# Kernel optimization log

Measured on AMD Instinct MI355X. Metric: run time of the kernel, lower is better.

## Reference

```python
import jax, jax.numpy as jnp
import numpy as np

B, T, D = 64, 512, 128          # batch, time, input_dim
S = 16                           # num_sessions
P, STRIDE = 3, 1                 # patch size / stride
H = 512                          # hidden_size
HORIZONS = (1, 5, 10)
K = len(HORIZONS)
TOK = D * P                      # token_dim = 384
EPS = 1e-6


def setup_inputs() -> dict:
    key = jax.random.key(0)
    ks = jax.random.split(key, 16)
    s = 0.02
    return {
        "x": jax.random.normal(ks[0], (B, T, D), jnp.float32),
        "session_idx": jax.random.randint(ks[1], (B,), 0, S),
        # per-session affine (expert) params
        "sess_W": jax.random.normal(ks[2], (S, D, D), jnp.float32) * s,
        "sess_b": jax.random.normal(ks[3], (S, D), jnp.float32) * s,
        # projection token_dim -> hidden
        "proj_W": jax.random.normal(ks[4], (H, TOK), jnp.float32) * s,
        "proj_b": jax.random.normal(ks[5], (H,), jnp.float32) * s,
        "rms_scale": jnp.ones((H,), jnp.float32),
        # single-layer GRU params (PyTorch layout: [3H, in], gate order r,z,n)
        "gru_Wih": jax.random.normal(ks[6], (3 * H, H), jnp.float32) * s,
        "gru_Whh": jax.random.normal(ks[7], (3 * H, H), jnp.float32) * s,
        "gru_bih": jax.random.normal(ks[8], (3 * H,), jnp.float32) * s,
        "gru_bhh": jax.random.normal(ks[9], (3 * H,), jnp.float32) * s,
        # future heads (K horizons): Linear(H,H) -> GELU -> Linear(H,TOK)
        "head_W1": jax.random.normal(ks[10], (K, H, H), jnp.float32) * s,
        "head_b1": jax.random.normal(ks[11], (K, H), jnp.float32) * s,
        "head_W2": jax.random.normal(ks[12], (K, TOK, H), jnp.float32) * s,
        "head_b2": jax.random.normal(ks[13], (K, TOK), jnp.float32) * s,
    }


def _forward(x, session_idx, sess_W, sess_b, proj_W, proj_b, rms_scale,
             gru_Wih, gru_Whh, gru_bih, gru_bhh,
             head_W1, head_b1, head_W2, head_b2):
    # --- per-sample session affine (expert gather + batched GEMM) ---
    W = sess_W[session_idx]                      # [B, D, D]
    b = sess_b[session_idx]                      # [B, D]
    aligned = jnp.einsum('btd,bed->bte', x, W) + b[:, None, :]  # y = x @ W.T + b

    # --- patch unfold along time; torch unfold gives [N, D, P] -> flatten (d,p) ---
    N = (T - P) // STRIDE + 1
    idx = jnp.arange(N)[:, None] * STRIDE + jnp.arange(P)[None, :]  # [N, P]
    win = aligned[:, idx, :]                     # [B, N, P, D]
    tokens = jnp.transpose(win, (0, 1, 3, 2)).reshape(B, N, TOK)    # [B, N, D*P]

    # --- projection + RMSNorm ---
    h = tokens @ proj_W.T + proj_b               # [B, N, H]
    rms = jnp.sqrt(jnp.mean(h * h, axis=-1, keepdims=True) + EPS)
    h = h / rms * rms_scale

    # --- GRU (PyTorch gate order r, z, n) via lax.scan over time ---
    gx = h @ gru_Wih.T + gru_bih                 # [B, N, 3H], precomputed input gates
    gx_t = jnp.transpose(gx, (1, 0, 2))          # [N, B, 3H]

    def step(hprev, g):
        gh = hprev @ gru_Whh.T + gru_bhh         # [B, 3H]
        r = jax.nn.sigmoid(g[:, :H] + gh[:, :H])
        z = jax.nn.sigmoid(g[:, H:2 * H] + gh[:, H:2 * H])
        n = jnp.tanh(g[:, 2 * H:] + r * gh[:, 2 * H:])
        hn = (1.0 - z) * n + z * hprev
        return hn, hn

    h0 = jnp.zeros((B, H), h.dtype)
    _, hs = jax.lax.scan(step, h0, gx_t)         # [N, B, H]
    hidden = jnp.transpose(hs, (1, 0, 2))        # [B, N, H]

    # --- multi-head future MLPs (stacked over K horizons) ---
    a = jnp.einsum('bnh,kfh->kbnf', hidden, head_W1) + head_b1[:, None, None, :]
    a = jax.nn.gelu(a, approximate=False)        # torch nn.GELU default = exact
    preds = jnp.einsum('kbnf,ktf->kbnt', a, head_W2) + head_b2[:, None, None, :]
    return preds, tokens                          # preds: [K, B, N, TOK]


def reference(x, session_idx, sess_W, sess_b, proj_W, proj_b, rms_scale,
              gru_Wih, gru_Whh, gru_bih, gru_bhh,
              head_W1, head_b1, head_W2, head_b2):
    return _forward(x, session_idx, sess_W, sess_b, proj_W, proj_b, rms_scale,
                    gru_Wih, gru_Whh, gru_bih, gru_bhh,
                    head_W1, head_b1, head_W2, head_b2)
```

## Files before the change

kernel.cpp:

```cpp
#include <hip/hip_runtime.h>
#include <hip/hip_bf16.h>
#include <math.h>

typedef __hip_bfloat16 bf16;
typedef __attribute__((ext_vector_type(8))) short short8;
typedef __attribute__((ext_vector_type(4))) short short4v;
typedef __attribute__((ext_vector_type(4))) float f32x4;

#define B_    64
#define T_    512
#define D_    128
#define N_    510
#define H_    512
#define TOK_  384
#define PRED1_ 12533760L
#define TOKOFF_ 37601280L

#define O_XBF  0UL
#define O_SWB  8388608UL
#define O_PW   8912896UL
#define O_WIH  9306112UL
#define O_WHH  10878976UL
#define O_W1   12451840UL
#define O_W2   14024704UL
#define O_TOK  15204352UL
#define O_HBF  40271872UL
#define O_HID  73695232UL
#define O_ABF  107118592UL
#define O_GX   140541952UL

__global__ void k_f2b(const float* __restrict__ s, bf16* __restrict__ d, int n4) {
  int i = blockIdx.x * 256 + threadIdx.x;
  if (i < n4) {
    float4 v = ((const float4*)s)[i];
    union { short4v sv; bf16 h[4]; } u;
    u.h[0] = __float2bfloat16(v.x); u.h[1] = __float2bfloat16(v.y);
    u.h[2] = __float2bfloat16(v.z); u.h[3] = __float2bfloat16(v.w);
    ((short4v*)d)[i] = u.sv;
  }
}

enum { EPI_F32 = 0, EPI_BF16 = 1, EPI_GELU = 2, EPI_TOK = 3, EPI_F32R = 4 };
#define SLDA 40

template <int EPI>
__global__ __launch_bounds__(256, 2) void k_gemm(
    const bf16* __restrict__ A, const bf16* __restrict__ W,
    const float* __restrict__ bias, void* __restrict__ C,
    int K, int ldc, long zA, long zW, long zB, long zC,
    const int* __restrict__ sidx, float* __restrict__ tokf, bf16* __restrict__ tokb)
{
  const int tid = threadIdx.x;
  const int bm = blockIdx.x, bn = blockIdx.y, z = blockIdx.z;
  const int wsel = (EPI == EPI_TOK) ? sidx[z] : z;
  const int lane = tid & 63, wave = tid >> 6;
  const int wm = (wave & 1) << 6, wn = (wave >> 1) << 6;
  const int r16 = lane & 15, quad = lane >> 4;

  __shared__ bf16 sA[128 * SLDA];
  __shared__ bf16 sB[128 * SLDA];

  const bf16* Ag = A + (long)z * zA + (long)bm * 128 * K;
  const bf16* Wg = W + (long)wsel * zW + (long)bn * 128 * K;

  f32x4 zf = {0.f, 0.f, 0.f, 0.f};
  f32x4 acc[4][4];
  for (int i = 0; i < 4; ++i) for (int j = 0; j < 4; ++j) acc[i][j] = zf;

  const int sr = tid >> 1, sc = (tid & 1) << 4;
  for (int k0 = 0; k0 < K; k0 += 32) {
    *(short8*)&sA[sr*SLDA + sc]     = *(const short8*)&Ag[(long)sr*K + k0 + sc];
    *(short8*)&sA[sr*SLDA + sc + 8] = *(const short8*)&Ag[(long)sr*K + k0 + sc + 8];
    *(short8*)&sB[sr*SLDA + sc]     = *(const short8*)&Wg[(long)sr*K + k0 + sc];
    *(short8*)&sB[sr*SLDA + sc + 8] = *(const short8*)&Wg[(long)sr*K + k0 + sc + 8];
    __syncthreads();
    short8 fa[4], fb[4];
    for (int i = 0; i < 4; ++i) fa[i] = *(const short8*)&sA[(wm + i*16 + r16)*SLDA + quad*8];
    for (int j = 0; j < 4; ++j) fb[j] = *(const short8*)&sB[(wn + j*16 + r16)*SLDA + quad*8];
    for (int i = 0; i < 4; ++i)
      for (int j = 0; j < 4; ++j)
        acc[i][j] = __builtin_amdgcn_mfma_f32_16x16x32_bf16(fa[i], fb[j], acc[i][j], 0, 0, 0);
    __syncthreads();
  }

  const float* bz = bias + (long)wsel * zB + bn * 128;
  for (int i = 0; i < 4; ++i) {
    for (int j = 0; j < 4; ++j) {
      const int colL = wn + j*16 + r16;
      const float bv = bz[colL];
      for (int r = 0; r < 4; ++r) {
        float v = acc[i][j][r] + bv;
        const long grow = (long)bm*128 + wm + i*16 + quad*4 + r;
        const long gcol = (long)bn*128 + colL;
        if (EPI == EPI_F32) {
          ((float*)C)[(long)z*zC + grow*ldc + gcol] = v;
        } else if (EPI == EPI_BF16) {
          ((bf16*)C)[(long)z*zC + grow*ldc + gcol] = __float2bfloat16(v);
        } else if (EPI == EPI_GELU) {
          v = 0.5f * v * (1.0f + erff(v * 0.70710678118654752f));
          ((bf16*)C)[(long)z*zC + grow*ldc + gcol] = __float2bfloat16(v);
        } else if (EPI == EPI_F32R) {
          const long rb = grow & 63, rn = grow >> 6;
          ((float*)C)[(rb*510 + rn)*ldc + gcol] = v;
        } else {
          for (int p = 0; p < 3; ++p) {
            long n = grow - p;
            if (n >= 0 && n < N_) {
              tokf[((long)z*N_ + n)*TOK_ + gcol*3 + p] = v;
              tokb[((long)n*B_ + z)*TOK_ + gcol*3 + p] = __float2bfloat16(v);
            }
          }
        }
      }
    }
  }
}

__global__ __launch_bounds__(256) void k_rms(const float* __restrict__ hpre,
                                             const float* __restrict__ scale,
                                             bf16* __restrict__ hbf)
{
  const int wave = threadIdx.x >> 6, lane = threadIdx.x & 63;
  const long row = (long)blockIdx.x * 4 + wave;
  const float* p = hpre + row * 512 + lane * 8;
  float4 v0 = *(const float4*)p;
  float4 v1 = *(const float4*)(p + 4);
  float ss = v0.x*v0.x + v0.y*v0.y + v0.z*v0.z + v0.w*v0.w
           + v1.x*v1.x + v1.y*v1.y + v1.z*v1.z + v1.w*v1.w;
  for (int m = 32; m >= 1; m >>= 1) ss += __shfl_xor(ss, m, 64);
  const float inv = 1.0f / sqrtf(ss * (1.0f/512.0f) + 1e-6f);
  const float* sc = scale + lane * 8;
  union { short8 sv; bf16 h[8]; } u;
  u.h[0] = __float2bfloat16(v0.x*inv*sc[0]); u.h[1] = __float2bfloat16(v0.y*inv*sc[1]);
  u.h[2] = __float2bfloat16(v0.z*inv*sc[2]); u.h[3] = __float2bfloat16(v0.w*inv*sc[3]);
  u.h[4] = __float2bfloat16(v1.x*inv*sc[4]); u.h[5] = __float2bfloat16(v1.y*inv*sc[5]);
  u.h[6] = __float2bfloat16(v1.z*inv*sc[6]); u.h[7] = __float2bfloat16(v1.w*inv*sc[7]);
  *(short8*)(hbf + row * 512 + lane * 8) = u.sv;
}

#define KP 520

#define GL2LDS(g, l) __builtin_amdgcn_global_load_lds( \
    (const __attribute__((address_space(1))) void*)(g), \
    (__attribute__((address_space(3))) void*)(l), 16, 0, 16)

__global__ __launch_bounds__(64, 1) void k_gru(
    const bf16* __restrict__ gx,
    const bf16* __restrict__ Whh,
    const float* __restrict__ bhh,
    bf16* __restrict__ hidden,
    int* __restrict__ flags)
{
  const int lane = threadIdx.x & 63;
  const int c16  = lane & 15, quad = lane >> 4;
  const int pw   = blockIdx.x & 31;
  const int gb   = blockIdx.x >> 5;
  const int hwv  = pw * 16;
  const int b0   = gb * 8;

  __shared__ bf16 wlds[16 * 3 * 64 * 8];
  __shared__ bf16 hp[8 * KP];

  for (int g3 = 0; g3 < 3; ++g3)
    for (int kt = 0; kt < 16; ++kt)
      *(short8*)&wlds[((kt*3 + g3)*64 + lane)*8] =
          *(const short8*)&Whh[(long)(g3*512 + hwv + c16)*512 + kt*32 + quad*8];
  const float bhr = bhh[       hwv + c16];
  const float bhz = bhh[ 512 + hwv + c16];
  const float bhn = bhh[1024 + hwv + c16];
  __syncthreads();

  int* myflag = &flags[(gb*32 + pw) * 32];
  const int pidx = (gb*32 + (lane & 31)) * 32;
  const int brv = (quad & 1) * 4;

  float gr[4], gz[4], gn[4];
  float hcur[4] = {0.f, 0.f, 0.f, 0.f};
  {
    const bf16* gxs = gx + (long)b0 * 1536 + hwv + c16;
#pragma unroll
    for (int i2 = 0; i2 < 4; ++i2) {
      const long ro = (long)(brv + i2) * 1536;
      gr[i2] = __bfloat162float(gxs[ro]);
      gz[i2] = __bfloat162float(gxs[ro + 512]);
      gn[i2] = __bfloat162float(gxs[ro + 1024]);
    }
  }

  for (int s = 0; s < 510; ++s) {
    f32x4 ar = {0.f,0.f,0.f,0.f}, az = {0.f,0.f,0.f,0.f}, an = {0.f,0.f,0.f,0.f};

    if (s > 0) {
      while (true) {
        int fv = __hip_atomic_load(&flags[pidx], __ATOMIC_RELAXED, __HIP_MEMORY_SCOPE_AGENT);
        if (__all(fv >= s)) break;
        __builtin_amdgcn_s_sleep(1);
      }
      asm volatile("" ::: "memory");

      const bf16* src = hidden + ((long)(s-1)*64 + b0)*512 + lane*8;
#pragma unroll
      for (int b = 0; b < 8; ++b) GL2LDS(src + b*512, &hp[b*KP]);
      asm volatile("s_waitcnt vmcnt(0)" ::: "memory");

#pragma unroll
      for (int kt = 0; kt < 16; ++kt) {
        short8 a  = *(const short8*)&hp[(c16 & 7)*KP + kt*32 + quad*8];
        short8 fr = *(const short8*)&wlds[((kt*3 + 0)*64 + lane)*8];
        short8 fz = *(const short8*)&wlds[((kt*3 + 1)*64 + lane)*8];
        short8 fn = *(const short8*)&wlds[((kt*3 + 2)*64 + lane)*8];
        ar = __builtin_amdgcn_mfma_f32_16x16x32_bf16(a, fr, ar, 0, 0, 0);
        az = __builtin_amdgcn_mfma_f32_16x16x32_bf16(a, fz, az, 0, 0, 0);
        an = __builtin_amdgcn_mfma_f32_16x16x32_bf16(a, fn, an, 0, 0, 0);
      }
    }

    if (quad < 2) {
#pragma unroll
      for (int i2 = 0; i2 < 4; ++i2) {
        const float r  = 1.0f / (1.0f + expf(-(gr[i2] + ar[i2] + bhr)));
        const float z  = 1.0f / (1.0f + expf(-(gz[i2] + az[i2] + bhz)));
        const float nn = tanhf(gn[i2] + r * (an[i2] + bhn));
        const float hn = (1.0f - z)*nn + z*hcur[i2];
        union { bf16 h; unsigned short u; } cb; cb.h = __float2bfloat16(hn);
        hcur[i2] = __bfloat162float(cb.h);
        unsigned mine = cb.u;
        unsigned part = (unsigned)__shfl_xor((int)mine, 1, 64);
        if (!(c16 & 1)) {
          unsigned w = (part << 16) | mine;
          __hip_atomic_store((unsigned*)(hidden + ((long)s*64 + b0 + brv + i2)*512 + hwv + c16),
                             w, __ATOMIC_RELAXED, __HIP_MEMORY_SCOPE_AGENT);
        }
      }
    }
    if (s < 509) {
      asm volatile("s_waitcnt vmcnt(0)" ::: "memory");
      if (lane == 0)
        __hip_atomic_store(myflag, s + 1, __ATOMIC_RELAXED, __HIP_MEMORY_SCOPE_AGENT);
      asm volatile("" ::: "memory");
      const bf16* gxs = gx + ((long)(s+1)*64 + b0)*1536 + hwv + c16;
#pragma unroll
      for (int i2 = 0; i2 < 4; ++i2) {
        const long ro = (long)(brv + i2) * 1536;
        gr[i2] = __bfloat162float(gxs[ro]);
        gz[i2] = __bfloat162float(gxs[ro + 512]);
        gn[i2] = __bfloat162float(gxs[ro + 1024]);
      }
    }
  }
}

extern "C" void kernel_launch(void* const* d_in, const int* in_sizes, int n_in,
                              void* d_out, int out_size, void* d_ws, size_t ws_size,
                              hipStream_t stream)
{
  const float* x    = (const float*)d_in[0];
  const int*   sidx = (const int*)d_in[1];
  const float* sW   = (const float*)d_in[2];
  const float* sb   = (const float*)d_in[3];
  const float* pW   = (const float*)d_in[4];
  const float* pb   = (const float*)d_in[5];
  const float* rsc  = (const float*)d_in[6];
  const float* wih  = (const float*)d_in[7];
  const float* whh  = (const float*)d_in[8];
  const float* bih  = (const float*)d_in[9];
  const float* bhh  = (const float*)d_in[10];
  const float* w1   = (const float*)d_in[11];
  const float* b1   = (const float*)d_in[12];
  const float* w2   = (const float*)d_in[13];
  const float* b2   = (const float*)d_in[14];
  char* ws = (char*)d_ws;
  float* out = (float*)d_out;

  bf16* xbf   = (bf16*)(ws + O_XBF);
  bf16* swbf  = (bf16*)(ws + O_SWB);
  bf16* pwbf  = (bf16*)(ws + O_PW);
  bf16* wihbf = (bf16*)(ws + O_WIH);
  bf16* whhbf = (bf16*)(ws + O_WHH);
  bf16* w1bf  = (bf16*)(ws + O_W1);
  bf16* w2bf  = (bf16*)(ws + O_W2);
  bf16* tokbf = (bf16*)(ws + O_TOK);
  bf16* hbf   = (bf16*)(ws + O_HBF);
  bf16* hidbf = (bf16*)(ws + O_HID);
  bf16* abf   = (bf16*)(ws + O_ABF);
  int*  bar   = (int*)(ws + O_ABF);
  float* hpre = (float*)(ws + O_GX);
  bf16* gxbf  = (bf16*)(ws + O_GX);

  auto cvt = [&](const float* s, bf16* dp, long n) {
    int n4 = (int)(n >> 2);
    k_f2b<<<dim3((n4 + 255) / 256), dim3(256), 0, stream>>>(s, dp, n4);
  };
  cvt(x,   xbf,   (long)B_*T_*D_);
  cvt(sW,  swbf,  16L*128*128);
  cvt(pW,  pwbf,  512L*384);
  cvt(wih, wihbf, 1536L*512);
  cvt(whh, whhbf, 1536L*512);
  cvt(w1,  w1bf,  3L*512*512);
  cvt(w2,  w2bf,  3L*384*512);

  k_gemm<EPI_TOK><<<dim3(4, 1, 64), dim3(256), 0, stream>>>(
      xbf, swbf, sb, nullptr, 128, 0,
      (long)T_*D_, 128L*128, 128L, 0L, sidx, out + TOKOFF_, tokbf);

  k_gemm<EPI_F32><<<dim3(255, 4, 1), dim3(256), 0, stream>>>(
      tokbf, pwbf, pb, hpre, 384, 512, 0, 0, 0, 0, nullptr, nullptr, nullptr);

  k_rms<<<dim3(8160), dim3(256), 0, stream>>>(hpre, rsc, hbf);

  k_gemm<EPI_BF16><<<dim3(255, 12, 1), dim3(256), 0, stream>>>(
      hbf, wihbf, bih, gxbf, 512, 1536, 0, 0, 0, 0, nullptr, nullptr, nullptr);

  hipMemsetAsync(ws + O_ABF, 0, 32768, stream);
  k_gru<<<dim3(256), dim3(64), 0, stream>>>(gxbf, whhbf, bhh, hidbf, bar);

  for (int k = 0; k < 3; ++k) {
    k_gemm<EPI_GELU><<<dim3(255, 4, 1), dim3(256), 0, stream>>>(
        hidbf, w1bf + (long)k*512*512, b1 + (long)k*512, abf,
        512, 512, 0, 0, 0, 0, nullptr, nullptr, nullptr);
    k_gemm<EPI_F32R><<<dim3(255, 3, 1), dim3(256), 0, stream>>>(
        abf, w2bf + (long)k*384*512, b2 + (long)k*384, out + (long)k*PRED1_,
        512, 384, 0, 0, 0, 0, nullptr, nullptr, nullptr);
  }
}
```

Measured before the change: 2.385 ms.

## Replace GRU flag barrier with sentinel-filled hidden buffer polling

Removes the per-step flag array and its store/poll handshake from the persistent GRU kernel. The hidden-state buffer is pre-filled with 0xFF sentinels, and each block re-loads the previous step's hidden rows into LDS until no sentinel pairs remain, then feeds them to the MFMAs. This cuts one global round trip and the vmcnt wait before each flag store from the serial recurrence. In exchange it adds a 33 MB memset per call. It also relies on the 32-bit hidden stores landing atomically and on a real bf16 pair never encoding 0xFFFFFFFF (NaN).

```diff
diff --git a/kernel.cpp b/kernel.cpp
--- a/kernel.cpp
+++ b/kernel.cpp
@@ -28,6 +28,8 @@
 #define O_HID  73695232UL
 #define O_ABF  107118592UL
 #define O_GX   140541952UL
+
+#define HID_BYTES 33423360UL
 
 __global__ void k_f2b(const float* __restrict__ s, bf16* __restrict__ d, int n4) {
   int i = blockIdx.x * 256 + threadIdx.x;
@@ -148,8 +150,7 @@
     const bf16* __restrict__ gx,
     const bf16* __restrict__ Whh,
     const float* __restrict__ bhh,
-    bf16* __restrict__ hidden,
-    int* __restrict__ flags)
+    bf16* __restrict__ hidden)
 {
   const int lane = threadIdx.x & 63;
   const int c16  = lane & 15, quad = lane >> 4;
@@ -170,8 +171,6 @@
   const float bhn = bhh[1024 + hwv + c16];
   __syncthreads();
 
-  int* myflag = &flags[(gb*32 + pw) * 32];
-  const int pidx = (gb*32 + (lane & 31)) * 32;
   const int brv = (quad & 1) * 4;
 
   float gr[4], gz[4], gn[4];
@@ -191,27 +190,32 @@
     f32x4 ar = {0.f,0.f,0.f,0.f}, az = {0.f,0.f,0.f,0.f}, an = {0.f,0.f,0.f,0.f};
 
     if (s > 0) {
+      union AU { unsigned u[4]; short8 s8; } au[16];
+      const bf16* src = hidden + ((long)(s-1)*64 + b0)*512 + lane*8;
       while (true) {
-        int fv = __hip_atomic_load(&flags[pidx], __ATOMIC_RELAXED, __HIP_MEMORY_SCOPE_AGENT);
-        if (__all(fv >= s)) break;
-        __builtin_amdgcn_s_sleep(1);
-      }
-      asm volatile("" ::: "memory");
-
-      const bf16* src = hidden + ((long)(s-1)*64 + b0)*512 + lane*8;
-#pragma unroll
-      for (int b = 0; b < 8; ++b) GL2LDS(src + b*512, &hp[b*KP]);
-      asm volatile("s_waitcnt vmcnt(0)" ::: "memory");
+#pragma unroll
+        for (int b = 0; b < 8; ++b) GL2LDS(src + b*512, &hp[b*KP]);
+        asm volatile("s_waitcnt vmcnt(0)" ::: "memory");
+        unsigned mx = 0u;
+#pragma unroll
+        for (int kt = 0; kt < 16; ++kt) {
+          au[kt].s8 = *(const short8*)&hp[(c16 & 7)*KP + kt*32 + quad*8];
+          unsigned m01 = au[kt].u[0] > au[kt].u[1] ? au[kt].u[0] : au[kt].u[1];
+          unsigned m23 = au[kt].u[2] > au[kt].u[3] ? au[kt].u[2] : au[kt].u[3];
+          unsigned m = m01 > m23 ? m01 : m23;
+          mx = mx > m ? mx : m;
+        }
+        if (__all(mx != 0xFFFFFFFFu)) break;
+      }
 
 #pragma unroll
       for (int kt = 0; kt < 16; ++kt) {
-        short8 a  = *(const short8*)&hp[(c16 & 7)*KP + kt*32 + quad*8];
         short8 fr = *(const short8*)&wlds[((kt*3 + 0)*64 + lane)*8];
         short8 fz = *(const short8*)&wlds[((kt*3 + 1)*64 + lane)*8];
         short8 fn = *(const short8*)&wlds[((kt*3 + 2)*64 + lane)*8];
-        ar = __builtin_amdgcn_mfma_f32_16x16x32_bf16(a, fr, ar, 0, 0, 0);
-        az = __builtin_amdgcn_mfma_f32_16x16x32_bf16(a, fz, az, 0, 0, 0);
-        an = __builtin_amdgcn_mfma_f32_16x16x32_bf16(a, fn, an, 0, 0, 0);
+        ar = __builtin_amdgcn_mfma_f32_16x16x32_bf16(au[kt].s8, fr, ar, 0, 0, 0);
+        az = __builtin_amdgcn_mfma_f32_16x16x32_bf16(au[kt].s8, fz, az, 0, 0, 0);
+        an = __builtin_amdgcn_mfma_f32_16x16x32_bf16(au[kt].s8, fn, an, 0, 0, 0);
       }
     }
 
@@ -234,9 +238,6 @@
       }
     }
     if (s < 509) {
-      asm volatile("s_waitcnt vmcnt(0)" ::: "memory");
-      if (lane == 0)
-        __hip_atomic_store(myflag, s + 1, __ATOMIC_RELAXED, __HIP_MEMORY_SCOPE_AGENT);
       asm volatile("" ::: "memory");
       const bf16* gxs = gx + ((long)(s+1)*64 + b0)*1536 + hwv + c16;
 #pragma unroll
@@ -283,9 +284,10 @@
   bf16* hbf   = (bf16*)(ws + O_HBF);
   bf16* hidbf = (bf16*)(ws + O_HID);
   bf16* abf   = (bf16*)(ws + O_ABF);
-  int*  bar   = (int*)(ws + O_ABF);
   float* hpre = (float*)(ws + O_GX);
   bf16* gxbf  = (bf16*)(ws + O_GX);
+
+  hipMemsetAsync(ws + O_HID, 0xFF, HID_BYTES, stream);
 
   auto cvt = [&](const float* s, bf16* dp, long n) {
     int n4 = (int)(n >> 2);
@@ -311,8 +313,7 @@
   k_gemm<EPI_BF16><<<dim3(255, 12, 1), dim3(256), 0, stream>>>(
       hbf, wihbf, bih, gxbf, 512, 1536, 0, 0, 0, 0, nullptr, nullptr, nullptr);
 
-  hipMemsetAsync(ws + O_ABF, 0, 32768, stream);
-  k_gru<<<dim3(256), dim3(64), 0, stream>>>(gxbf, whhbf, bhh, hidbf, bar);
+  k_gru<<<dim3(256), dim3(64), 0, stream>>>(gxbf, whhbf, bhh, hidbf);
 
   for (int k = 0; k < 3; ++k) {
     k_gemm<EPI_GELU><<<dim3(255, 4, 1), dim3(256), 0, stream>>>(
```

After: 2.115 ms, median of 2. -11.3%, faster.
